# Optimization experiments

Hardware: AMD Instinct MI355X
Metric: run time of the kernel (lower is better)

## Reference

```python
import jax, jax.numpy as jnp
import numpy as np

A = 10      # n_trained_players = n_trained_off(5) + n_trained_def(5)
T = 65      # timesteps; scan runs T-1 = 64 steps
B = 128     # batch
XD, YD, ZD, HD, MD, RM = 2, 20, 64, 256, 90, 256
LOG2PI = float(np.log(2.0 * np.pi))


def _lin(x, W, b):
    # batched per-agent linear: x [A,B,in], W [A,in,out], b [A,out]
    return jnp.einsum('abi,aio->abo', x, W) + b[:, None, :]


def _mlp2(x, W1, b1, W2, b2):
    return jax.nn.relu(_lin(jax.nn.relu(_lin(x, W1, b1)), W2, b2))


def setup_inputs() -> dict:
    key = jax.random.key(0)
    ks = jax.random.split(key, 40)
    s = 0.05
    def w(i, shape):
        return jax.random.normal(ks[i], shape, dtype=jnp.float32) * s
    enc_in, pri_in, dec_in, gru_in = XD + MD + RM, MD + RM, YD + MD + ZD + RM, XD + ZD
    inp = {
        'data': jax.random.normal(ks[0], (T, B, YD), dtype=jnp.float32),
        'macro': jax.random.randint(ks[1], (T, B, A), 0, MD),
        'eps': jax.random.normal(ks[2], (T - 1, A, B, ZD), dtype=jnp.float32),
        'enc_W1': w(3, (A, enc_in, HD)), 'enc_b1': w(4, (A, HD)),
        'enc_W2': w(5, (A, HD, HD)), 'enc_b2': w(6, (A, HD)),
        'encm_W': w(7, (A, HD, ZD)), 'encm_b': w(8, (A, ZD)),
        'encs_W': w(9, (A, HD, ZD)), 'encs_b': w(10, (A, ZD)),
        'pri_W1': w(11, (A, pri_in, HD)), 'pri_b1': w(12, (A, HD)),
        'pri_W2': w(13, (A, HD, HD)), 'pri_b2': w(14, (A, HD)),
        'prim_W': w(15, (A, HD, ZD)), 'prim_b': w(16, (A, ZD)),
        'pris_W': w(17, (A, HD, ZD)), 'pris_b': w(18, (A, ZD)),
        'dec_W1': w(19, (A, dec_in, HD)), 'dec_b1': w(20, (A, HD)),
        'dec_W2': w(21, (A, HD, HD)), 'dec_b2': w(22, (A, HD)),
        'decm_W': w(23, (A, HD, XD)), 'decm_b': w(24, (A, XD)),
        'decs_W': w(25, (A, HD, XD)), 'decs_b': w(26, (A, XD)),
        'gru_Wih': w(27, (A, gru_in, 3 * RM)), 'gru_bih': w(28, (A, 3 * RM)),
        'gru_Whh': w(29, (A, RM, 3 * RM)), 'gru_bhh': w(30, (A, 3 * RM)),
    }
    return inp


def _forward(data, macro, eps, enc_W1, enc_b1, enc_W2, enc_b2, encm_W, encm_b,
             encs_W, encs_b, pri_W1, pri_b1, pri_W2, pri_b2, prim_W, prim_b,
             pris_W, pris_b, dec_W1, dec_b1, dec_W2, dec_b2, decm_W, decm_b,
             decs_W, decs_b, gru_Wih, gru_bih, gru_Whh, gru_bhh):
    # x: next-step per-player positions [T-1, A, B, 2]
    x = data[1:].reshape(T - 1, B, A, XD).transpose(0, 2, 1, 3)
    # macro one-hot, [T, A, B, 90]
    m = jax.nn.one_hot(macro, MD, dtype=data.dtype).transpose(0, 2, 1, 3)
    h0 = jnp.zeros((A, B, RM), data.dtype)
    zero = jnp.zeros((), data.dtype)

    def step(carry, ts):
        h, recon, kl = carry
        x_t, y_t, m_t, e_t = ts  # [A,B,2], [B,20], [A,B,90], [A,B,ZD]
        yb = jnp.broadcast_to(y_t[None], (A, B, YD))
        # encoder q(z|x,m,h)
        enc_h = _mlp2(jnp.concatenate([x_t, m_t, h], -1), enc_W1, enc_b1, enc_W2, enc_b2)
        enc_mean = _lin(enc_h, encm_W, encm_b)
        enc_std = jax.nn.softplus(_lin(enc_h, encs_W, encs_b))
        # prior p(z|m,h)
        pri_h = _mlp2(jnp.concatenate([m_t, h], -1), pri_W1, pri_b1, pri_W2, pri_b2)
        pri_mean = _lin(pri_h, prim_W, prim_b)
        pri_std = jax.nn.softplus(_lin(pri_h, pris_W, pris_b))
        # reparameterized sample
        z_t = enc_mean + e_t * enc_std
        # decoder p(x|y,m,z,h)
        dec_h = _mlp2(jnp.concatenate([yb, m_t, z_t, h], -1), dec_W1, dec_b1, dec_W2, dec_b2)
        dec_mean = _lin(dec_h, decm_W, decm_b)
        dec_std = jax.nn.softplus(_lin(dec_h, decs_W, decs_b))
        # per-agent 1-layer GRU (torch gate order: reset, update, new)
        gi = _lin(jnp.concatenate([x_t, z_t], -1), gru_Wih, gru_bih)
        gh = _lin(h, gru_Whh, gru_bhh)
        ir, iz, inn = jnp.split(gi, 3, axis=-1)
        hr, hz, hn = jnp.split(gh, 3, axis=-1)
        r = jax.nn.sigmoid(ir + hr)
        u = jax.nn.sigmoid(iz + hz)
        n = jnp.tanh(inn + r * hn)
        h_new = (1.0 - u) * n + u * h
        # losses (summed over all agents/batch/dims, as in torch code)
        kl = kl + 0.5 * jnp.sum(2.0 * jnp.log(pri_std) - 2.0 * jnp.log(enc_std)
                                + (enc_std ** 2 + (enc_mean - pri_mean) ** 2) / pri_std ** 2 - 1.0)
        recon = recon + jnp.sum(0.5 * ((x_t - dec_mean) / dec_std) ** 2
                                + jnp.log(dec_std) + 0.5 * LOG2PI)
        return (h_new, recon, kl), None

    xs = (x, data[:-1], m[:-1], eps)
    (_, recon, kl), _ = jax.lax.scan(step, (h0, zero, zero), xs)
    return recon, kl


def reference(data, macro, eps, enc_W1, enc_b1, enc_W2, enc_b2, encm_W, encm_b,
              encs_W, encs_b, pri_W1, pri_b1, pri_W2, pri_b2, prim_W, prim_b,
              pris_W, pris_b, dec_W1, dec_b1, dec_W2, dec_b2, decm_W, decm_b,
              decs_W, decs_b, gru_Wih, gru_bih, gru_Whh, gru_bhh):
    return _forward(data, macro, eps, enc_W1, enc_b1, enc_W2, enc_b2, encm_W, encm_b,
                    encs_W, encs_b, pri_W1, pri_b1, pri_W2, pri_b2, prim_W, prim_b,
                    pris_W, pris_b, dec_W1, dec_b1, dec_W2, dec_b2, decm_W, decm_b,
                    decs_W, decs_b, gru_Wih, gru_bih, gru_Whh, gru_bhh)
```

## Files before the change

kernel.cpp:

```cpp
#include <hip/hip_runtime.h>
#include <math.h>

#define NA 10
#define NT 65
#define NB 128
#define XDIM 2
#define YDIM 20
#define ZDIM 64
#define HDIM 256
#define RMDIM 256
#define NSTEP 64
#define TS 8
#define HR (TS + 1)
#define LOG2PI 1.8378770664093453f

#define ENC_W1_S (348 * 256)
#define PRI_W1_S (346 * 256)
#define DEC_W1_S (430 * 256)
#define GRU_WIH_S (66 * 768)
#define GRU_WHH_S (256 * 768)
#define W2_S (256 * 256)
#define HEADW_S (256 * 64)

#define SA (256 * NB)
#define GA (768 * NB)
#define ZA (ZDIM * NB)

static __device__ __forceinline__ float sp(float x) {
    return fmaxf(x, 0.f) + log1pf(expf(-fabsf(x)));
}
static __device__ __forceinline__ float sigm(float x) { return 1.f / (1.f + expf(-x)); }
static __device__ __forceinline__ float relu(float x) { return fmaxf(x, 0.f); }

__global__ __launch_bounds__(256) void k_init(float* __restrict__ h0, double* __restrict__ accd) {
    int i = blockIdx.x * 256 + threadIdx.x;
    ((float4*)h0)[i] = make_float4(0.f, 0.f, 0.f, 0.f);
    if (i == 0) {
        accd[0] = 0.0;
        accd[1] = 0.0;
    }
}

__global__ __launch_bounds__(256) void kS1(const float* __restrict__ h,
                                           const float* __restrict__ enc_W1,
                                           const float* __restrict__ enc_b1,
                                           const float* __restrict__ pri_W1,
                                           const float* __restrict__ pri_b1,
                                           const float* __restrict__ gru_Whh,
                                           const float* __restrict__ gru_bhh,
                                           const float* __restrict__ data,
                                           const int* __restrict__ macro, float* __restrict__ ench1,
                                           float* __restrict__ prih1, float* __restrict__ ghB,
                                           int t) {
    int tid = threadIdx.x, bid = blockIdx.x;
    int lane = tid & 63, wv = tid >> 6;
    int a = bid / 80;
    int r = bid % 80;
    int b0 = (r & 1) * 64;
    int tile = r >> 1;
    int ep, c0;
    const float* Wb;
    int wld;
    if (tile < 8) {
        ep = 0; c0 = tile * 32;
        Wb = enc_W1 + a * ENC_W1_S + 92 * 256; wld = 256;
    } else if (tile < 16) {
        ep = 1; c0 = (tile - 8) * 32;
        Wb = pri_W1 + a * PRI_W1_S + 90 * 256; wld = 256;
    } else {
        ep = 2; c0 = (tile - 16) * 32;
        Wb = gru_Whh + a * GRU_WHH_S; wld = 768;
    }
    int n0u = __builtin_amdgcn_readfirstlane(c0 + wv * 8);
    int row = b0 + lane;
    const float* X = h + a * SA + row;
    const float* wp = Wb + n0u;
    float acc[8] = {};
#pragma unroll 8
    for (int k = 0; k < 256; ++k) {
        float xv = X[k * NB];
        const float* wr = wp + k * wld;
#pragma unroll
        for (int j = 0; j < 8; ++j) acc[j] = fmaf(xv, wr[j], acc[j]);
    }
    if (ep == 2) {
#pragma unroll
        for (int j = 0; j < 8; ++j) {
            float v = acc[j] + gru_bhh[a * 768 + n0u + j];
            ghB[a * GA + (n0u + j) * NB + row] = v;
        }
    } else {
        const float* W1b = (ep == 0) ? enc_W1 + a * ENC_W1_S : pri_W1 + a * PRI_W1_S;
        const float* bb = (ep == 0) ? enc_b1 + a * HDIM : pri_b1 + a * HDIM;
        int mi = macro[(t * NB + row) * NA + a];
        const float* mrow = W1b + (ep == 0 ? 2 + mi : mi) * 256;
        float xv0 = 0.f, xv1 = 0.f;
        if (ep == 0) {
            xv0 = data[(t + 1) * (NB * YDIM) + row * YDIM + a * XDIM];
            xv1 = data[(t + 1) * (NB * YDIM) + row * YDIM + a * XDIM + 1];
        }
        float* outp = (ep == 0) ? ench1 : prih1;
#pragma unroll
        for (int j = 0; j < 8; ++j) {
            float v = acc[j] + bb[n0u + j] + mrow[n0u + j];
            if (ep == 0) v += xv0 * W1b[n0u + j] + xv1 * W1b[256 + n0u + j];
            outp[a * SA + (n0u + j) * NB + row] = relu(v);
        }
    }
}

__global__ __launch_bounds__(256) void kS2(const float* __restrict__ ench1,
                                           const float* __restrict__ prih1,
                                           const float* __restrict__ enc_W2,
                                           const float* __restrict__ enc_b2,
                                           const float* __restrict__ pri_W2,
                                           const float* __restrict__ pri_b2,
                                           float* __restrict__ ench2, float* __restrict__ prih2) {
    int tid = threadIdx.x, bid = blockIdx.x;
    int lane = tid & 63, wv = tid >> 6;
    int a = bid / 32;
    int r = bid % 32;
    int isenc = (r < 16);
    int q = isenc ? r : r - 16;
    int b0 = (q & 1) * 64;
    int c0 = (q >> 1) * 32;
    int n0u = __builtin_amdgcn_readfirstlane(c0 + wv * 8);
    int row = b0 + lane;
    const float* X = (isenc ? ench1 : prih1) + a * SA + row;
    const float* wp = (isenc ? enc_W2 : pri_W2) + a * W2_S + n0u;
    const float* bb = (isenc ? enc_b2 : pri_b2) + a * HDIM;
    float acc[8] = {};
#pragma unroll 8
    for (int k = 0; k < 256; ++k) {
        float xv = X[k * NB];
        const float* wr = wp + k * 256;
#pragma unroll
        for (int j = 0; j < 8; ++j) acc[j] = fmaf(xv, wr[j], acc[j]);
    }
    float* outp = isenc ? ench2 : prih2;
#pragma unroll
    for (int j = 0; j < 8; ++j)
        outp[a * SA + (n0u + j) * NB + row] = relu(acc[j] + bb[n0u + j]);
}

__global__ __launch_bounds__(256) void kS3(const float* __restrict__ ench2,
                                           const float* __restrict__ prih2,
                                           const float* __restrict__ encm_W,
                                           const float* __restrict__ encm_b,
                                           const float* __restrict__ encs_W,
                                           const float* __restrict__ encs_b,
                                           const float* __restrict__ prim_W,
                                           const float* __restrict__ prim_b,
                                           const float* __restrict__ pris_W,
                                           const float* __restrict__ pris_b,
                                           const float* __restrict__ eps, float* __restrict__ z_t,
                                           double* __restrict__ accd, int t) {
    __shared__ float L[4][16][64];
    __shared__ float red[256];
    int tid = threadIdx.x, bid = blockIdx.x;
    int lane = tid & 63, wv = tid >> 6;
    int a = bid / 8;
    int r = bid % 8;
    int b0 = (r & 1) * 64;
    int zc0 = (r >> 1) * 16;
    int row = b0 + lane;
    const float* Wt;
    const float* Bt;
    if (wv == 0) { Wt = encm_W; Bt = encm_b; }
    else if (wv == 1) { Wt = encs_W; Bt = encs_b; }
    else if (wv == 2) { Wt = prim_W; Bt = prim_b; }
    else { Wt = pris_W; Bt = pris_b; }
    const float* X = (wv < 2 ? ench2 : prih2) + a * SA + row;
    const float* wp = Wt + a * HEADW_S + zc0;
    float acc[16] = {};
#pragma unroll 4
    for (int k = 0; k < 256; ++k) {
        float xv = X[k * NB];
        const float* wr = wp + k * ZDIM;
#pragma unroll
        for (int j = 0; j < 16; ++j) acc[j] = fmaf(xv, wr[j], acc[j]);
    }
#pragma unroll
    for (int j = 0; j < 16; ++j) L[wv][j][lane] = acc[j] + Bt[a * ZDIM + zc0 + j];
    __syncthreads();
    float part = 0.f;
#pragma unroll
    for (int q = 0; q < 4; ++q) {
        int zc = wv * 4 + q;
        float em = L[0][zc][lane];
        float es = sp(L[1][zc][lane]);
        float pm = L[2][zc][lane];
        float ps = sp(L[3][zc][lane]);
        float ev = eps[((t * NA + a) * NB + row) * ZDIM + zc0 + zc];
        z_t[a * ZA + (zc0 + zc) * NB + row] = em + ev * es;
        float dm = em - pm;
        part += 0.5f * (2.f * logf(ps) - 2.f * logf(es) + (es * es + dm * dm) / (ps * ps) - 1.f);
    }
    red[tid] = part;
    __syncthreads();
#pragma unroll
    for (int s = 128; s > 0; s >>= 1) {
        if (tid < s) red[tid] += red[tid + s];
        __syncthreads();
    }
    if (tid == 0) atomicAdd(&accd[1], (double)red[0]);
}

__global__ __launch_bounds__(256) void kS4(const float* __restrict__ z_t,
                                           const float* __restrict__ data,
                                           const float* __restrict__ gru_Wih,
                                           const float* __restrict__ gru_bih,
                                           const float* __restrict__ ghB,
                                           const float* __restrict__ h_t, float* __restrict__ h_nx,
                                           int t) {
    int tid = threadIdx.x, bid = blockIdx.x;
    int lane = tid & 63, wv = tid >> 6;
    int a = bid / 16;
    int r = bid % 16;
    int b0 = (r & 1) * 64;
    int c0 = (r >> 1) * 32;
    int n0u = __builtin_amdgcn_readfirstlane(c0 + wv * 8);
    int row = b0 + lane;
    const float* X = z_t + a * ZA + row;
    const float* wp = gru_Wih + a * GRU_WIH_S + 2 * 768 + n0u;
    float acc[3][8] = {};
#pragma unroll 8
    for (int k = 0; k < 64; ++k) {
        float xv = X[k * NB];
        const float* wr = wp + k * 768;
#pragma unroll
        for (int j = 0; j < 8; ++j) acc[0][j] = fmaf(xv, wr[j], acc[0][j]);
#pragma unroll
        for (int j = 0; j < 8; ++j) acc[1][j] = fmaf(xv, wr[256 + j], acc[1][j]);
#pragma unroll
        for (int j = 0; j < 8; ++j) acc[2][j] = fmaf(xv, wr[512 + j], acc[2][j]);
    }
    float xv0 = data[(t + 1) * (NB * YDIM) + row * YDIM + a * XDIM];
    float xv1 = data[(t + 1) * (NB * YDIM) + row * YDIM + a * XDIM + 1];
    const float* Wih0 = gru_Wih + a * GRU_WIH_S;
    const float* bih = gru_bih + a * 768;
    const float* ghb = ghB + a * GA + row;
    const float* hb = h_t + a * SA + row;
    float* ob = h_nx + a * SA + row;
#pragma unroll
    for (int j = 0; j < 8; ++j) {
        int cr = n0u + j;
        float gi0 = acc[0][j] + bih[cr] + xv0 * Wih0[cr] + xv1 * Wih0[768 + cr];
        float gi1 = acc[1][j] + bih[256 + cr] + xv0 * Wih0[256 + cr] + xv1 * Wih0[768 + 256 + cr];
        float gi2 = acc[2][j] + bih[512 + cr] + xv0 * Wih0[512 + cr] + xv1 * Wih0[768 + 512 + cr];
        float hrv = ghb[cr * NB];
        float hzv = ghb[(256 + cr) * NB];
        float hnv = ghb[(512 + cr) * NB];
        float hov = hb[cr * NB];
        float rr = sigm(gi0 + hrv);
        float uu = sigm(gi1 + hzv);
        float nn = tanhf(gi2 + rr * hnv);
        ob[cr * NB] = (1.f - uu) * nn + uu * hov;
    }
}

__global__ __launch_bounds__(256) void kDec1(const float* __restrict__ data,
                                             const int* __restrict__ macro,
                                             const float* __restrict__ z_ring,
                                             const float* __restrict__ h_ring,
                                             const float* __restrict__ dec_W1,
                                             const float* __restrict__ dec_b1,
                                             float* __restrict__ dech1s, int t0) {
    int tid = threadIdx.x, bid = blockIdx.x;
    int lane = tid & 63, wv = tid >> 6;
    int ti = bid / 160;
    int rem = bid % 160;
    int a = rem / 16;
    int r = rem % 16;
    int b0 = (r & 1) * 64;
    int c0 = (r >> 1) * 32;
    int t = t0 + ti;
    int n0u = __builtin_amdgcn_readfirstlane(c0 + wv * 8);
    int row = b0 + lane;
    const float* Wb = dec_W1 + a * DEC_W1_S;
    const float* wp = Wb + n0u;
    float acc[8] = {};
    const float* yrow = data + t * (NB * YDIM) + row * YDIM;
#pragma unroll 4
    for (int k = 0; k < YDIM; ++k) {
        float xv = yrow[k];
        const float* wr = wp + k * 256;
#pragma unroll
        for (int j = 0; j < 8; ++j) acc[j] = fmaf(xv, wr[j], acc[j]);
    }
    const float* Xz = z_ring + (size_t)(t % TS) * (NA * ZA) + a * ZA + row;
#pragma unroll 8
    for (int k = 0; k < ZDIM; ++k) {
        float xv = Xz[k * NB];
        const float* wr = wp + (110 + k) * 256;
#pragma unroll
        for (int j = 0; j < 8; ++j) acc[j] = fmaf(xv, wr[j], acc[j]);
    }
    const float* Xh = h_ring + (size_t)(t % HR) * (NA * SA) + a * SA + row;
#pragma unroll 8
    for (int k = 0; k < 256; ++k) {
        float xv = Xh[k * NB];
        const float* wr = wp + (174 + k) * 256;
#pragma unroll
        for (int j = 0; j < 8; ++j) acc[j] = fmaf(xv, wr[j], acc[j]);
    }
    int mi = macro[(t * NB + row) * NA + a];
    const float* mrow = Wb + (20 + mi) * 256;
    const float* bb = dec_b1 + a * HDIM;
    float* ob = dech1s + (size_t)(ti * NA + a) * SA + row;
#pragma unroll
    for (int j = 0; j < 8; ++j)
        ob[(n0u + j) * NB] = relu(acc[j] + bb[n0u + j] + mrow[n0u + j]);
}

__global__ __launch_bounds__(256) void kDec2(const float* __restrict__ dech1s,
                                             const float* __restrict__ dec_W2,
                                             const float* __restrict__ dec_b2,
                                             float* __restrict__ dech2s) {
    int tid = threadIdx.x, bid = blockIdx.x;
    int lane = tid & 63, wv = tid >> 6;
    int ti = bid / 160;
    int rem = bid % 160;
    int a = rem / 16;
    int r = rem % 16;
    int b0 = (r & 1) * 64;
    int c0 = (r >> 1) * 32;
    int n0u = __builtin_amdgcn_readfirstlane(c0 + wv * 8);
    int row = b0 + lane;
    const float* X = dech1s + (size_t)(ti * NA + a) * SA + row;
    const float* wp = dec_W2 + a * W2_S + n0u;
    const float* bb = dec_b2 + a * HDIM;
    float acc[8] = {};
#pragma unroll 8
    for (int k = 0; k < 256; ++k) {
        float xv = X[k * NB];
        const float* wr = wp + k * 256;
#pragma unroll
        for (int j = 0; j < 8; ++j) acc[j] = fmaf(xv, wr[j], acc[j]);
    }
    float* ob = dech2s + (size_t)(ti * NA + a) * SA + row;
#pragma unroll
    for (int j = 0; j < 8; ++j)
        ob[(n0u + j) * NB] = relu(acc[j] + bb[n0u + j]);
}

__global__ __launch_bounds__(256) void kEpi(const float* __restrict__ dech2s,
                                            const float* __restrict__ decm_W,
                                            const float* __restrict__ decm_b,
                                            const float* __restrict__ decs_W,
                                            const float* __restrict__ decs_b,
                                            const float* __restrict__ data,
                                            double* __restrict__ accd, int t0) {
    int tid = threadIdx.x;
    int widx = blockIdx.x * 4 + (tid >> 6);
    int lane = tid & 63;
    int ti = widx / 1280;
    int rem = widx - ti * 1280;
    int a = rem >> 7, b = rem & 127;
    int targ = t0 + ti + 1;
    const float* dbase = dech2s + (size_t)(ti * NA + a) * SA + b;
    float hv0 = dbase[(lane * 4 + 0) * NB];
    float hv1 = dbase[(lane * 4 + 1) * NB];
    float hv2 = dbase[(lane * 4 + 2) * NB];
    float hv3 = dbase[(lane * 4 + 3) * NB];
    const float* wmb = decm_W + a * (HDIM * XDIM) + lane * 8;
    const float4 wm0 = *(const float4*)&wmb[0];
    const float4 wm1 = *(const float4*)&wmb[4];
    const float* wsb = decs_W + a * (HDIM * XDIM) + lane * 8;
    const float4 ws0 = *(const float4*)&wsb[0];
    const float4 ws1 = *(const float4*)&wsb[4];
    float m0 = hv0 * wm0.x + hv1 * wm0.z + hv2 * wm1.x + hv3 * wm1.z;
    float m1 = hv0 * wm0.y + hv1 * wm0.w + hv2 * wm1.y + hv3 * wm1.w;
    float s0 = hv0 * ws0.x + hv1 * ws0.z + hv2 * ws1.x + hv3 * ws1.z;
    float s1 = hv0 * ws0.y + hv1 * ws0.w + hv2 * ws1.y + hv3 * ws1.w;
#pragma unroll
    for (int off = 32; off > 0; off >>= 1) {
        m0 += __shfl_down(m0, off, 64);
        m1 += __shfl_down(m1, off, 64);
        s0 += __shfl_down(s0, off, 64);
        s1 += __shfl_down(s1, off, 64);
    }
    if (lane == 0) {
        float dm0 = m0 + decm_b[a * 2 + 0];
        float dm1 = m1 + decm_b[a * 2 + 1];
        float ds0 = sp(s0 + decs_b[a * 2 + 0]);
        float ds1 = sp(s1 + decs_b[a * 2 + 1]);
        float x0 = data[targ * (NB * YDIM) + b * YDIM + a * XDIM + 0];
        float x1 = data[targ * (NB * YDIM) + b * YDIM + a * XDIM + 1];
        float r0 = (x0 - dm0) / ds0, r1 = (x1 - dm1) / ds1;
        float tt = 0.5f * r0 * r0 + logf(ds0) + 0.5f * LOG2PI + 0.5f * r1 * r1 + logf(ds1) +
                   0.5f * LOG2PI;
        atomicAdd(&accd[0], (double)tt);
    }
}

__global__ void k_final(const double* __restrict__ accd, float* __restrict__ out) {
    if (threadIdx.x == 0) {
        out[0] = (float)accd[0];
        out[1] = (float)accd[1];
    }
}

extern "C" void kernel_launch(void* const* d_in, const int* in_sizes, int n_in, void* d_out,
                              int out_size, void* d_ws, size_t ws_size, hipStream_t stream) {
    const float* data = (const float*)d_in[0];
    const int* macro = (const int*)d_in[1];
    const float* eps = (const float*)d_in[2];
    const float* enc_W1 = (const float*)d_in[3];
    const float* enc_b1 = (const float*)d_in[4];
    const float* enc_W2 = (const float*)d_in[5];
    const float* enc_b2 = (const float*)d_in[6];
    const float* encm_W = (const float*)d_in[7];
    const float* encm_b = (const float*)d_in[8];
    const float* encs_W = (const float*)d_in[9];
    const float* encs_b = (const float*)d_in[10];
    const float* pri_W1 = (const float*)d_in[11];
    const float* pri_b1 = (const float*)d_in[12];
    const float* pri_W2 = (const float*)d_in[13];
    const float* pri_b2 = (const float*)d_in[14];
    const float* prim_W = (const float*)d_in[15];
    const float* prim_b = (const float*)d_in[16];
    const float* pris_W = (const float*)d_in[17];
    const float* pris_b = (const float*)d_in[18];
    const float* dec_W1 = (const float*)d_in[19];
    const float* dec_b1 = (const float*)d_in[20];
    const float* dec_W2 = (const float*)d_in[21];
    const float* dec_b2 = (const float*)d_in[22];
    const float* decm_W = (const float*)d_in[23];
    const float* decm_b = (const float*)d_in[24];
    const float* decs_W = (const float*)d_in[25];
    const float* decs_b = (const float*)d_in[26];
    const float* gru_Wih = (const float*)d_in[27];
    const float* gru_bih = (const float*)d_in[28];
    const float* gru_Whh = (const float*)d_in[29];
    const float* gru_bhh = (const float*)d_in[30];

    double* accd = (double*)d_ws;
    float* base = (float*)((char*)d_ws + 256);
    float* h_ring = base;
    float* z_ring = h_ring + (size_t)HR * NA * SA;
    float* ench1 = z_ring + (size_t)TS * NA * ZA;
    float* prih1 = ench1 + NA * SA;
    float* ench2 = prih1 + NA * SA;
    float* prih2 = ench2 + NA * SA;
    float* ghB = prih2 + NA * SA;
    float* dech1s = ghB + NA * GA;
    float* dech2s = dech1s + (size_t)TS * NA * SA;
    float* out = (float*)d_out;

    k_init<<<320, 256, 0, stream>>>(h_ring, accd);
    for (int t = 0; t < NSTEP; ++t) {
        float* h_t = h_ring + (size_t)(t % HR) * NA * SA;
        float* h_nx = h_ring + (size_t)((t + 1) % HR) * NA * SA;
        float* z_t = z_ring + (size_t)(t % TS) * NA * ZA;
        kS1<<<800, 256, 0, stream>>>(h_t, enc_W1, enc_b1, pri_W1, pri_b1, gru_Whh, gru_bhh, data,
                                     macro, ench1, prih1, ghB, t);
        kS2<<<320, 256, 0, stream>>>(ench1, prih1, enc_W2, enc_b2, pri_W2, pri_b2, ench2, prih2);
        kS3<<<80, 256, 0, stream>>>(ench2, prih2, encm_W, encm_b, encs_W, encs_b, prim_W, prim_b,
                                    pris_W, pris_b, eps, z_t, accd, t);
        kS4<<<160, 256, 0, stream>>>(z_t, data, gru_Wih, gru_bih, ghB, h_t, h_nx, t);
        if ((t % TS) == TS - 1) {
            int t0 = t - TS + 1;
            kDec1<<<TS * 160, 256, 0, stream>>>(data, macro, z_ring, h_ring, dec_W1, dec_b1,
                                                dech1s, t0);
            kDec2<<<TS * 160, 256, 0, stream>>>(dech1s, dec_W2, dec_b2, dech2s);
            kEpi<<<TS * 320, 256, 0, stream>>>(dech2s, decm_W, decm_b, decs_W, decs_b, data, accd,
                                               t0);
        }
    }
    k_final<<<1, 64, 0, stream>>>(accd, out);
}
```

Before: 11.29 ms.

## Replace per-step kernel launches with one persistent cooperative kernel using grid syncs

Merges all per-timestep kernels into a single cooperative persistent kernel that walks task lists and separates stages with grid-wide barriers, removing about 260 kernel launches. The decoder path is software-pipelined so each decoder step runs eight steps behind the scan, alongside scan work in the same phases, instead of in batched bursts. The latent heads are split into their own phase so more blocks share that work. The cost is grid.sync overhead per phase and occupancy limits from running a persistent grid.

```diff
diff --git a/kernel.cpp b/kernel.cpp
--- a/kernel.cpp
+++ b/kernel.cpp
@@ -1,5 +1,8 @@
 #include <hip/hip_runtime.h>
+#include <hip/hip_cooperative_groups.h>
 #include <math.h>
+
+namespace cg = cooperative_groups;
 
 #define NA 10
 #define NT 65
@@ -12,6 +15,7 @@
 #define NSTEP 64
 #define TS 8
 #define HR (TS + 1)
+#define MAXTASK 980
 #define LOG2PI 1.8378770664093453f
 
 #define ENC_W1_S (348 * 256)
@@ -32,30 +36,24 @@
 static __device__ __forceinline__ float sigm(float x) { return 1.f / (1.f + expf(-x)); }
 static __device__ __forceinline__ float relu(float x) { return fmaxf(x, 0.f); }
 
-__global__ __launch_bounds__(256) void k_init(float* __restrict__ h0, double* __restrict__ accd) {
-    int i = blockIdx.x * 256 + threadIdx.x;
-    ((float4*)h0)[i] = make_float4(0.f, 0.f, 0.f, 0.f);
-    if (i == 0) {
-        accd[0] = 0.0;
-        accd[1] = 0.0;
-    }
-}
-
-__global__ __launch_bounds__(256) void kS1(const float* __restrict__ h,
-                                           const float* __restrict__ enc_W1,
-                                           const float* __restrict__ enc_b1,
-                                           const float* __restrict__ pri_W1,
-                                           const float* __restrict__ pri_b1,
-                                           const float* __restrict__ gru_Whh,
-                                           const float* __restrict__ gru_bhh,
-                                           const float* __restrict__ data,
-                                           const int* __restrict__ macro, float* __restrict__ ench1,
-                                           float* __restrict__ prih1, float* __restrict__ ghB,
-                                           int t) {
-    int tid = threadIdx.x, bid = blockIdx.x;
-    int lane = tid & 63, wv = tid >> 6;
-    int a = bid / 80;
-    int r = bid % 80;
+struct Prm {
+    const float* data;
+    const int* macro;
+    const float* eps;
+    const float *enc_W1, *enc_b1, *enc_W2, *enc_b2, *encm_W, *encm_b, *encs_W, *encs_b;
+    const float *pri_W1, *pri_b1, *pri_W2, *pri_b2, *prim_W, *prim_b, *pris_W, *pris_b;
+    const float *dec_W1, *dec_b1, *dec_W2, *dec_b2, *decm_W, *decm_b, *decs_W, *decs_b;
+    const float *gWih, *gbih, *gWhh, *gbhh;
+    float *h_ring, *z_ring, *e1, *p1, *e2, *p2, *heads, *ghB, *dech1, *dech2;
+    double* accd;
+    float* out;
+};
+
+static __device__ __forceinline__ void task_l1(const Prm& p, int id, int t, const float* h_t) {
+    int tid = threadIdx.x;
+    int lane = tid & 63, wv = tid >> 6;
+    int a = id / 80;
+    int r = id % 80;
     int b0 = (r & 1) * 64;
     int tile = r >> 1;
     int ep, c0;
@@ -63,17 +61,17 @@
     int wld;
     if (tile < 8) {
         ep = 0; c0 = tile * 32;
-        Wb = enc_W1 + a * ENC_W1_S + 92 * 256; wld = 256;
+        Wb = p.enc_W1 + a * ENC_W1_S + 92 * 256; wld = 256;
     } else if (tile < 16) {
         ep = 1; c0 = (tile - 8) * 32;
-        Wb = pri_W1 + a * PRI_W1_S + 90 * 256; wld = 256;
+        Wb = p.pri_W1 + a * PRI_W1_S + 90 * 256; wld = 256;
     } else {
         ep = 2; c0 = (tile - 16) * 32;
-        Wb = gru_Whh + a * GRU_WHH_S; wld = 768;
-    }
-    int n0u = __builtin_amdgcn_readfirstlane(c0 + wv * 8);
-    int row = b0 + lane;
-    const float* X = h + a * SA + row;
+        Wb = p.gWhh + a * GRU_WHH_S; wld = 768;
+    }
+    int n0u = __builtin_amdgcn_readfirstlane(c0 + wv * 8);
+    int row = b0 + lane;
+    const float* X = h_t + a * SA + row;
     const float* wp = Wb + n0u;
     float acc[8] = {};
 #pragma unroll 8
@@ -85,21 +83,19 @@
     }
     if (ep == 2) {
 #pragma unroll
-        for (int j = 0; j < 8; ++j) {
-            float v = acc[j] + gru_bhh[a * 768 + n0u + j];
-            ghB[a * GA + (n0u + j) * NB + row] = v;
-        }
+        for (int j = 0; j < 8; ++j)
+            p.ghB[a * GA + (n0u + j) * NB + row] = acc[j] + p.gbhh[a * 768 + n0u + j];
     } else {
-        const float* W1b = (ep == 0) ? enc_W1 + a * ENC_W1_S : pri_W1 + a * PRI_W1_S;
-        const float* bb = (ep == 0) ? enc_b1 + a * HDIM : pri_b1 + a * HDIM;
-        int mi = macro[(t * NB + row) * NA + a];
+        const float* W1b = (ep == 0) ? p.enc_W1 + a * ENC_W1_S : p.pri_W1 + a * PRI_W1_S;
+        const float* bb = (ep == 0) ? p.enc_b1 + a * HDIM : p.pri_b1 + a * HDIM;
+        int mi = p.macro[(t * NB + row) * NA + a];
         const float* mrow = W1b + (ep == 0 ? 2 + mi : mi) * 256;
         float xv0 = 0.f, xv1 = 0.f;
         if (ep == 0) {
-            xv0 = data[(t + 1) * (NB * YDIM) + row * YDIM + a * XDIM];
-            xv1 = data[(t + 1) * (NB * YDIM) + row * YDIM + a * XDIM + 1];
-        }
-        float* outp = (ep == 0) ? ench1 : prih1;
+            xv0 = p.data[(t + 1) * (NB * YDIM) + row * YDIM + a * XDIM];
+            xv1 = p.data[(t + 1) * (NB * YDIM) + row * YDIM + a * XDIM + 1];
+        }
+        float* outp = (ep == 0) ? p.e1 : p.p1;
 #pragma unroll
         for (int j = 0; j < 8; ++j) {
             float v = acc[j] + bb[n0u + j] + mrow[n0u + j];
@@ -109,26 +105,111 @@
     }
 }
 
-__global__ __launch_bounds__(256) void kS2(const float* __restrict__ ench1,
-                                           const float* __restrict__ prih1,
-                                           const float* __restrict__ enc_W2,
-                                           const float* __restrict__ enc_b2,
-                                           const float* __restrict__ pri_W2,
-                                           const float* __restrict__ pri_b2,
-                                           float* __restrict__ ench2, float* __restrict__ prih2) {
-    int tid = threadIdx.x, bid = blockIdx.x;
-    int lane = tid & 63, wv = tid >> 6;
-    int a = bid / 32;
-    int r = bid % 32;
-    int isenc = (r < 16);
-    int q = isenc ? r : r - 16;
+static __device__ __forceinline__ void task_dec1(const Prm& p, int q, int tD) {
+    int tid = threadIdx.x;
+    int lane = tid & 63, wv = tid >> 6;
+    int a = q / 16;
+    int r = q % 16;
+    int b0 = (r & 1) * 64;
+    int c0 = (r >> 1) * 32;
+    int n0u = __builtin_amdgcn_readfirstlane(c0 + wv * 8);
+    int row = b0 + lane;
+    const float* Wb = p.dec_W1 + a * DEC_W1_S;
+    const float* wp = Wb + n0u;
+    float acc[8] = {};
+    const float* yrow = p.data + tD * (NB * YDIM) + row * YDIM;
+#pragma unroll 4
+    for (int k = 0; k < YDIM; ++k) {
+        float xv = yrow[k];
+        const float* wr = wp + k * 256;
+#pragma unroll
+        for (int j = 0; j < 8; ++j) acc[j] = fmaf(xv, wr[j], acc[j]);
+    }
+    const float* Xz = p.z_ring + (size_t)(tD % TS) * (NA * ZA) + a * ZA + row;
+#pragma unroll 8
+    for (int k = 0; k < ZDIM; ++k) {
+        float xv = Xz[k * NB];
+        const float* wr = wp + (110 + k) * 256;
+#pragma unroll
+        for (int j = 0; j < 8; ++j) acc[j] = fmaf(xv, wr[j], acc[j]);
+    }
+    const float* Xh = p.h_ring + (size_t)(tD % HR) * (NA * SA) + a * SA + row;
+#pragma unroll 8
+    for (int k = 0; k < 256; ++k) {
+        float xv = Xh[k * NB];
+        const float* wr = wp + (174 + k) * 256;
+#pragma unroll
+        for (int j = 0; j < 8; ++j) acc[j] = fmaf(xv, wr[j], acc[j]);
+    }
+    int mi = p.macro[(tD * NB + row) * NA + a];
+    const float* mrow = Wb + (20 + mi) * 256;
+    const float* bb = p.dec_b1 + a * HDIM;
+    float* ob = p.dech1 + a * SA + row;
+#pragma unroll
+    for (int j = 0; j < 8; ++j)
+        ob[(n0u + j) * NB] = relu(acc[j] + bb[n0u + j] + mrow[n0u + j]);
+}
+
+static __device__ __forceinline__ void task_epi(const Prm& p, int q, int tE, float* Ls) {
+    int tid = threadIdx.x;
+    int lane = tid & 63, wv = tid >> 6;
+    int a = q >> 1;
     int b0 = (q & 1) * 64;
-    int c0 = (q >> 1) * 32;
-    int n0u = __builtin_amdgcn_readfirstlane(c0 + wv * 8);
-    int row = b0 + lane;
-    const float* X = (isenc ? ench1 : prih1) + a * SA + row;
-    const float* wp = (isenc ? enc_W2 : pri_W2) + a * W2_S + n0u;
-    const float* bb = (isenc ? enc_b2 : pri_b2) + a * HDIM;
+    int row = b0 + lane;
+    const float* d2 = p.dech2 + a * SA;
+    const float* wm = p.decm_W + a * (HDIM * XDIM);
+    const float* ws = p.decs_W + a * (HDIM * XDIM);
+    float m0 = 0.f, m1 = 0.f, s0 = 0.f, s1 = 0.f;
+#pragma unroll 8
+    for (int kk = 0; kk < 64; ++kk) {
+        int k = wv * 64 + kk;
+        float xv = d2[k * NB + row];
+        m0 = fmaf(xv, wm[k * 2], m0);
+        m1 = fmaf(xv, wm[k * 2 + 1], m1);
+        s0 = fmaf(xv, ws[k * 2], s0);
+        s1 = fmaf(xv, ws[k * 2 + 1], s1);
+    }
+    Ls[(wv * 4 + 0) * 64 + lane] = m0;
+    Ls[(wv * 4 + 1) * 64 + lane] = m1;
+    Ls[(wv * 4 + 2) * 64 + lane] = s0;
+    Ls[(wv * 4 + 3) * 64 + lane] = s1;
+    __syncthreads();
+    if (wv == 0) {
+        float M0 = Ls[0 * 64 + lane] + Ls[4 * 64 + lane] + Ls[8 * 64 + lane] + Ls[12 * 64 + lane];
+        float M1 = Ls[1 * 64 + lane] + Ls[5 * 64 + lane] + Ls[9 * 64 + lane] + Ls[13 * 64 + lane];
+        float S0 = Ls[2 * 64 + lane] + Ls[6 * 64 + lane] + Ls[10 * 64 + lane] + Ls[14 * 64 + lane];
+        float S1 = Ls[3 * 64 + lane] + Ls[7 * 64 + lane] + Ls[11 * 64 + lane] + Ls[15 * 64 + lane];
+        float dm0 = M0 + p.decm_b[a * 2 + 0];
+        float dm1 = M1 + p.decm_b[a * 2 + 1];
+        float ds0 = sp(S0 + p.decs_b[a * 2 + 0]);
+        float ds1 = sp(S1 + p.decs_b[a * 2 + 1]);
+        int targ = tE + 1;
+        float x0 = p.data[targ * (NB * YDIM) + row * YDIM + a * XDIM + 0];
+        float x1 = p.data[targ * (NB * YDIM) + row * YDIM + a * XDIM + 1];
+        float r0 = (x0 - dm0) / ds0, r1 = (x1 - dm1) / ds1;
+        float tt = 0.5f * r0 * r0 + logf(ds0) + 0.5f * LOG2PI + 0.5f * r1 * r1 + logf(ds1) +
+                   0.5f * LOG2PI;
+#pragma unroll
+        for (int off = 32; off > 0; off >>= 1) tt += __shfl_down(tt, off, 64);
+        if (lane == 0) atomicAdd(&p.accd[0], (double)tt);
+    }
+    __syncthreads();
+}
+
+static __device__ __forceinline__ void task_l2(const Prm& p, int id) {
+    int tid = threadIdx.x;
+    int lane = tid & 63, wv = tid >> 6;
+    int isenc = (id < 160);
+    int q = isenc ? id : id - 160;
+    int a = q / 16;
+    int r = q % 16;
+    int b0 = (r & 1) * 64;
+    int c0 = (r >> 1) * 32;
+    int n0u = __builtin_amdgcn_readfirstlane(c0 + wv * 8);
+    int row = b0 + lane;
+    const float* X = (isenc ? p.e1 : p.p1) + a * SA + row;
+    const float* wp = (isenc ? p.enc_W2 : p.pri_W2) + a * W2_S + n0u;
+    const float* bb = (isenc ? p.enc_b2 : p.pri_b2) + a * HDIM;
     float acc[8] = {};
 #pragma unroll 8
     for (int k = 0; k < 256; ++k) {
@@ -137,96 +218,118 @@
 #pragma unroll
         for (int j = 0; j < 8; ++j) acc[j] = fmaf(xv, wr[j], acc[j]);
     }
-    float* outp = isenc ? ench2 : prih2;
+    float* outp = isenc ? p.e2 : p.p2;
 #pragma unroll
     for (int j = 0; j < 8; ++j)
         outp[a * SA + (n0u + j) * NB + row] = relu(acc[j] + bb[n0u + j]);
 }
 
-__global__ __launch_bounds__(256) void kS3(const float* __restrict__ ench2,
-                                           const float* __restrict__ prih2,
-                                           const float* __restrict__ encm_W,
-                                           const float* __restrict__ encm_b,
-                                           const float* __restrict__ encs_W,
-                                           const float* __restrict__ encs_b,
-                                           const float* __restrict__ prim_W,
-                                           const float* __restrict__ prim_b,
-                                           const float* __restrict__ pris_W,
-                                           const float* __restrict__ pris_b,
-                                           const float* __restrict__ eps, float* __restrict__ z_t,
-                                           double* __restrict__ accd, int t) {
-    __shared__ float L[4][16][64];
-    __shared__ float red[256];
-    int tid = threadIdx.x, bid = blockIdx.x;
-    int lane = tid & 63, wv = tid >> 6;
-    int a = bid / 8;
-    int r = bid % 8;
-    int b0 = (r & 1) * 64;
-    int zc0 = (r >> 1) * 16;
-    int row = b0 + lane;
+static __device__ __forceinline__ void task_dec2(const Prm& p, int q) {
+    int tid = threadIdx.x;
+    int lane = tid & 63, wv = tid >> 6;
+    int a = q / 16;
+    int r = q % 16;
+    int b0 = (r & 1) * 64;
+    int c0 = (r >> 1) * 32;
+    int n0u = __builtin_amdgcn_readfirstlane(c0 + wv * 8);
+    int row = b0 + lane;
+    const float* X = p.dech1 + a * SA + row;
+    const float* wp = p.dec_W2 + a * W2_S + n0u;
+    const float* bb = p.dec_b2 + a * HDIM;
+    float acc[8] = {};
+#pragma unroll 8
+    for (int k = 0; k < 256; ++k) {
+        float xv = X[k * NB];
+        const float* wr = wp + k * 256;
+#pragma unroll
+        for (int j = 0; j < 8; ++j) acc[j] = fmaf(xv, wr[j], acc[j]);
+    }
+    float* ob = p.dech2 + a * SA + row;
+#pragma unroll
+    for (int j = 0; j < 8; ++j)
+        ob[(n0u + j) * NB] = relu(acc[j] + bb[n0u + j]);
+}
+
+static __device__ __forceinline__ void task_heads(const Prm& p, int id) {
+    int tid = threadIdx.x;
+    int lane = tid & 63, wv = tid >> 6;
+    int a = id / 16;
+    int r = id % 16;
+    int b0 = (r & 1) * 64;
+    int hc = r >> 1;
+    int head = hc >> 1, c0 = (hc & 1) * 32;
     const float* Wt;
     const float* Bt;
-    if (wv == 0) { Wt = encm_W; Bt = encm_b; }
-    else if (wv == 1) { Wt = encs_W; Bt = encs_b; }
-    else if (wv == 2) { Wt = prim_W; Bt = prim_b; }
-    else { Wt = pris_W; Bt = pris_b; }
-    const float* X = (wv < 2 ? ench2 : prih2) + a * SA + row;
-    const float* wp = Wt + a * HEADW_S + zc0;
-    float acc[16] = {};
-#pragma unroll 4
+    if (head == 0) { Wt = p.encm_W; Bt = p.encm_b; }
+    else if (head == 1) { Wt = p.encs_W; Bt = p.encs_b; }
+    else if (head == 2) { Wt = p.prim_W; Bt = p.prim_b; }
+    else { Wt = p.pris_W; Bt = p.pris_b; }
+    int n0u = __builtin_amdgcn_readfirstlane(c0 + wv * 8);
+    int row = b0 + lane;
+    const float* X = (head < 2 ? p.e2 : p.p2) + a * SA + row;
+    const float* wp = Wt + a * HEADW_S + n0u;
+    float acc[8] = {};
+#pragma unroll 8
     for (int k = 0; k < 256; ++k) {
         float xv = X[k * NB];
         const float* wr = wp + k * ZDIM;
 #pragma unroll
-        for (int j = 0; j < 16; ++j) acc[j] = fmaf(xv, wr[j], acc[j]);
-    }
-#pragma unroll
-    for (int j = 0; j < 16; ++j) L[wv][j][lane] = acc[j] + Bt[a * ZDIM + zc0 + j];
+        for (int j = 0; j < 8; ++j) acc[j] = fmaf(xv, wr[j], acc[j]);
+    }
+#pragma unroll
+    for (int j = 0; j < 8; ++j)
+        p.heads[a * SA + (head * 64 + n0u + j) * NB + row] = acc[j] + Bt[a * ZDIM + n0u + j];
+}
+
+static __device__ __forceinline__ void task_p4(const Prm& p, int id, int t, const float* h_t,
+                                               float* h_nx, float* z_t, float* Ls, float* red) {
+    int tid = threadIdx.x;
+    int lane = tid & 63, wv = tid >> 6;
+    int a = id / 16;
+    int r = id % 16;
+    int b0 = (r & 1) * 64;
+    int c0 = (r >> 1) * 32;
+    int n0u = __builtin_amdgcn_readfirstlane(c0 + wv * 8);
+    const float* heads_a = p.heads + a * SA;
+    {
+        int rl = tid & 63, zg = tid >> 6;
+        int rg = b0 + rl;
+        float part = 0.f;
+#pragma unroll 4
+        for (int i = 0; i < 16; ++i) {
+            int zc = zg * 16 + i;
+            float em = heads_a[zc * NB + rg];
+            float esr = heads_a[(64 + zc) * NB + rg];
+            float es = sp(esr);
+            float e = p.eps[((size_t)(t * NA + a) * NB + rg) * ZDIM + zc];
+            float zv = em + e * es;
+            Ls[zc * 64 + rl] = zv;
+            if (c0 == 0) z_t[a * ZA + zc * NB + rg] = zv;
+            if (c0 == 32) {
+                float pm = heads_a[(128 + zc) * NB + rg];
+                float ps = sp(heads_a[(192 + zc) * NB + rg]);
+                float dm = em - pm;
+                part += 0.5f * (2.f * logf(ps) - 2.f * logf(es) +
+                                (es * es + dm * dm) / (ps * ps) - 1.f);
+            }
+        }
+        if (c0 == 32) red[tid] = part;
+    }
     __syncthreads();
-    float part = 0.f;
-#pragma unroll
-    for (int q = 0; q < 4; ++q) {
-        int zc = wv * 4 + q;
-        float em = L[0][zc][lane];
-        float es = sp(L[1][zc][lane]);
-        float pm = L[2][zc][lane];
-        float ps = sp(L[3][zc][lane]);
-        float ev = eps[((t * NA + a) * NB + row) * ZDIM + zc0 + zc];
-        z_t[a * ZA + (zc0 + zc) * NB + row] = em + ev * es;
-        float dm = em - pm;
-        part += 0.5f * (2.f * logf(ps) - 2.f * logf(es) + (es * es + dm * dm) / (ps * ps) - 1.f);
-    }
-    red[tid] = part;
-    __syncthreads();
-#pragma unroll
-    for (int s = 128; s > 0; s >>= 1) {
-        if (tid < s) red[tid] += red[tid + s];
+    if (c0 == 32) {
+#pragma unroll
+        for (int s = 128; s > 0; s >>= 1) {
+            if (tid < s) red[tid] += red[tid + s];
+            __syncthreads();
+        }
+        if (tid == 0) atomicAdd(&p.accd[1], (double)red[0]);
         __syncthreads();
     }
-    if (tid == 0) atomicAdd(&accd[1], (double)red[0]);
-}
-
-__global__ __launch_bounds__(256) void kS4(const float* __restrict__ z_t,
-                                           const float* __restrict__ data,
-                                           const float* __restrict__ gru_Wih,
-                                           const float* __restrict__ gru_bih,
-                                           const float* __restrict__ ghB,
-                                           const float* __restrict__ h_t, float* __restrict__ h_nx,
-                                           int t) {
-    int tid = threadIdx.x, bid = blockIdx.x;
-    int lane = tid & 63, wv = tid >> 6;
-    int a = bid / 16;
-    int r = bid % 16;
-    int b0 = (r & 1) * 64;
-    int c0 = (r >> 1) * 32;
-    int n0u = __builtin_amdgcn_readfirstlane(c0 + wv * 8);
-    int row = b0 + lane;
-    const float* X = z_t + a * ZA + row;
-    const float* wp = gru_Wih + a * GRU_WIH_S + 2 * 768 + n0u;
     float acc[3][8] = {};
+    const float* wp = p.gWih + a * GRU_WIH_S + 2 * 768 + n0u;
 #pragma unroll 8
     for (int k = 0; k < 64; ++k) {
-        float xv = X[k * NB];
+        float xv = Ls[k * 64 + lane];
         const float* wr = wp + k * 768;
 #pragma unroll
         for (int j = 0; j < 8; ++j) acc[0][j] = fmaf(xv, wr[j], acc[0][j]);
@@ -235,11 +338,12 @@
 #pragma unroll
         for (int j = 0; j < 8; ++j) acc[2][j] = fmaf(xv, wr[512 + j], acc[2][j]);
     }
-    float xv0 = data[(t + 1) * (NB * YDIM) + row * YDIM + a * XDIM];
-    float xv1 = data[(t + 1) * (NB * YDIM) + row * YDIM + a * XDIM + 1];
-    const float* Wih0 = gru_Wih + a * GRU_WIH_S;
-    const float* bih = gru_bih + a * 768;
-    const float* ghb = ghB + a * GA + row;
+    int row = b0 + lane;
+    float xv0 = p.data[(t + 1) * (NB * YDIM) + row * YDIM + a * XDIM];
+    float xv1 = p.data[(t + 1) * (NB * YDIM) + row * YDIM + a * XDIM + 1];
+    const float* Wih0 = p.gWih + a * GRU_WIH_S;
+    const float* bih = p.gbih + a * 768;
+    const float* ghb = p.ghB + a * GA + row;
     const float* hb = h_t + a * SA + row;
     float* ob = h_nx + a * SA + row;
 #pragma unroll
@@ -257,216 +361,113 @@
         float nn = tanhf(gi2 + rr * hnv);
         ob[cr * NB] = (1.f - uu) * nn + uu * hov;
     }
-}
-
-__global__ __launch_bounds__(256) void kDec1(const float* __restrict__ data,
-                                             const int* __restrict__ macro,
-                                             const float* __restrict__ z_ring,
-                                             const float* __restrict__ h_ring,
-                                             const float* __restrict__ dec_W1,
-                                             const float* __restrict__ dec_b1,
-                                             float* __restrict__ dech1s, int t0) {
-    int tid = threadIdx.x, bid = blockIdx.x;
-    int lane = tid & 63, wv = tid >> 6;
-    int ti = bid / 160;
-    int rem = bid % 160;
-    int a = rem / 16;
-    int r = rem % 16;
-    int b0 = (r & 1) * 64;
-    int c0 = (r >> 1) * 32;
-    int t = t0 + ti;
-    int n0u = __builtin_amdgcn_readfirstlane(c0 + wv * 8);
-    int row = b0 + lane;
-    const float* Wb = dec_W1 + a * DEC_W1_S;
-    const float* wp = Wb + n0u;
-    float acc[8] = {};
-    const float* yrow = data + t * (NB * YDIM) + row * YDIM;
-#pragma unroll 4
-    for (int k = 0; k < YDIM; ++k) {
-        float xv = yrow[k];
-        const float* wr = wp + k * 256;
-#pragma unroll
-        for (int j = 0; j < 8; ++j) acc[j] = fmaf(xv, wr[j], acc[j]);
-    }
-    const float* Xz = z_ring + (size_t)(t % TS) * (NA * ZA) + a * ZA + row;
-#pragma unroll 8
-    for (int k = 0; k < ZDIM; ++k) {
-        float xv = Xz[k * NB];
-        const float* wr = wp + (110 + k) * 256;
-#pragma unroll
-        for (int j = 0; j < 8; ++j) acc[j] = fmaf(xv, wr[j], acc[j]);
-    }
-    const float* Xh = h_ring + (size_t)(t % HR) * (NA * SA) + a * SA + row;
-#pragma unroll 8
-    for (int k = 0; k < 256; ++k) {
-        float xv = Xh[k * NB];
-        const float* wr = wp + (174 + k) * 256;
-#pragma unroll
-        for (int j = 0; j < 8; ++j) acc[j] = fmaf(xv, wr[j], acc[j]);
-    }
-    int mi = macro[(t * NB + row) * NA + a];
-    const float* mrow = Wb + (20 + mi) * 256;
-    const float* bb = dec_b1 + a * HDIM;
-    float* ob = dech1s + (size_t)(ti * NA + a) * SA + row;
-#pragma unroll
-    for (int j = 0; j < 8; ++j)
-        ob[(n0u + j) * NB] = relu(acc[j] + bb[n0u + j] + mrow[n0u + j]);
-}
-
-__global__ __launch_bounds__(256) void kDec2(const float* __restrict__ dech1s,
-                                             const float* __restrict__ dec_W2,
-                                             const float* __restrict__ dec_b2,
-                                             float* __restrict__ dech2s) {
-    int tid = threadIdx.x, bid = blockIdx.x;
-    int lane = tid & 63, wv = tid >> 6;
-    int ti = bid / 160;
-    int rem = bid % 160;
-    int a = rem / 16;
-    int r = rem % 16;
-    int b0 = (r & 1) * 64;
-    int c0 = (r >> 1) * 32;
-    int n0u = __builtin_amdgcn_readfirstlane(c0 + wv * 8);
-    int row = b0 + lane;
-    const float* X = dech1s + (size_t)(ti * NA + a) * SA + row;
-    const float* wp = dec_W2 + a * W2_S + n0u;
-    const float* bb = dec_b2 + a * HDIM;
-    float acc[8] = {};
-#pragma unroll 8
-    for (int k = 0; k < 256; ++k) {
-        float xv = X[k * NB];
-        const float* wr = wp + k * 256;
-#pragma unroll
-        for (int j = 0; j < 8; ++j) acc[j] = fmaf(xv, wr[j], acc[j]);
-    }
-    float* ob = dech2s + (size_t)(ti * NA + a) * SA + row;
-#pragma unroll
-    for (int j = 0; j < 8; ++j)
-        ob[(n0u + j) * NB] = relu(acc[j] + bb[n0u + j]);
-}
-
-__global__ __launch_bounds__(256) void kEpi(const float* __restrict__ dech2s,
-                                            const float* __restrict__ decm_W,
-                                            const float* __restrict__ decm_b,
-                                            const float* __restrict__ decs_W,
-                                            const float* __restrict__ decs_b,
-                                            const float* __restrict__ data,
-                                            double* __restrict__ accd, int t0) {
-    int tid = threadIdx.x;
-    int widx = blockIdx.x * 4 + (tid >> 6);
-    int lane = tid & 63;
-    int ti = widx / 1280;
-    int rem = widx - ti * 1280;
-    int a = rem >> 7, b = rem & 127;
-    int targ = t0 + ti + 1;
-    const float* dbase = dech2s + (size_t)(ti * NA + a) * SA + b;
-    float hv0 = dbase[(lane * 4 + 0) * NB];
-    float hv1 = dbase[(lane * 4 + 1) * NB];
-    float hv2 = dbase[(lane * 4 + 2) * NB];
-    float hv3 = dbase[(lane * 4 + 3) * NB];
-    const float* wmb = decm_W + a * (HDIM * XDIM) + lane * 8;
-    const float4 wm0 = *(const float4*)&wmb[0];
-    const float4 wm1 = *(const float4*)&wmb[4];
-    const float* wsb = decs_W + a * (HDIM * XDIM) + lane * 8;
-    const float4 ws0 = *(const float4*)&wsb[0];
-    const float4 ws1 = *(const float4*)&wsb[4];
-    float m0 = hv0 * wm0.x + hv1 * wm0.z + hv2 * wm1.x + hv3 * wm1.z;
-    float m1 = hv0 * wm0.y + hv1 * wm0.w + hv2 * wm1.y + hv3 * wm1.w;
-    float s0 = hv0 * ws0.x + hv1 * ws0.z + hv2 * ws1.x + hv3 * ws1.z;
-    float s1 = hv0 * ws0.y + hv1 * ws0.w + hv2 * ws1.y + hv3 * ws1.w;
-#pragma unroll
-    for (int off = 32; off > 0; off >>= 1) {
-        m0 += __shfl_down(m0, off, 64);
-        m1 += __shfl_down(m1, off, 64);
-        s0 += __shfl_down(s0, off, 64);
-        s1 += __shfl_down(s1, off, 64);
-    }
-    if (lane == 0) {
-        float dm0 = m0 + decm_b[a * 2 + 0];
-        float dm1 = m1 + decm_b[a * 2 + 1];
-        float ds0 = sp(s0 + decs_b[a * 2 + 0]);
-        float ds1 = sp(s1 + decs_b[a * 2 + 1]);
-        float x0 = data[targ * (NB * YDIM) + b * YDIM + a * XDIM + 0];
-        float x1 = data[targ * (NB * YDIM) + b * YDIM + a * XDIM + 1];
-        float r0 = (x0 - dm0) / ds0, r1 = (x1 - dm1) / ds1;
-        float tt = 0.5f * r0 * r0 + logf(ds0) + 0.5f * LOG2PI + 0.5f * r1 * r1 + logf(ds1) +
-                   0.5f * LOG2PI;
-        atomicAdd(&accd[0], (double)tt);
-    }
-}
-
-__global__ void k_final(const double* __restrict__ accd, float* __restrict__ out) {
-    if (threadIdx.x == 0) {
-        out[0] = (float)accd[0];
-        out[1] = (float)accd[1];
+    __syncthreads();
+}
+
+__global__ __launch_bounds__(256, 4) void kmain(Prm p) {
+    cg::grid_group grid = cg::this_grid();
+    const int tid = threadIdx.x, bid = blockIdx.x;
+    const int nb = gridDim.x;
+    __shared__ float Ls[64 * 64];
+    __shared__ float red[256];
+    {
+        int g0 = bid * 256 + tid;
+        float4* h0 = (float4*)p.h_ring;
+        for (int i = g0; i < (NA * SA) / 4; i += nb * 256)
+            h0[i] = make_float4(0.f, 0.f, 0.f, 0.f);
+        if (g0 == 0) { p.accd[0] = 0.0; p.accd[1] = 0.0; }
+    }
+    grid.sync();
+    for (int t = 0; t <= NSTEP + 8; ++t) {
+        const float* h_t = p.h_ring + (size_t)(t % HR) * NA * SA;
+        float* h_nx = p.h_ring + (size_t)((t + 1) % HR) * NA * SA;
+        float* z_t = p.z_ring + (size_t)(t % TS) * NA * ZA;
+        int tD = t - 8, tE = t - 9;
+        int nScan = (t < NSTEP) ? 800 : 0;
+        int nD1 = (tD >= 0 && tD < NSTEP) ? 160 : 0;
+        int nEpi = (tE >= 0 && tE < NSTEP) ? 20 : 0;
+        for (int id = bid; id < nScan + nD1 + nEpi; id += nb) {
+            if (id < nScan) task_l1(p, id, t, h_t);
+            else if (id < nScan + nD1) task_dec1(p, id - nScan, tD);
+            else task_epi(p, id - nScan - nD1, tE, Ls);
+        }
+        grid.sync();
+        int nL2 = (t < NSTEP) ? 320 : 0;
+        int nD2 = nD1;
+        for (int id = bid; id < nL2 + nD2; id += nb) {
+            if (id < nL2) task_l2(p, id);
+            else task_dec2(p, id - nL2);
+        }
+        grid.sync();
+        if (t < NSTEP) {
+            for (int id = bid; id < 160; id += nb) task_heads(p, id);
+            grid.sync();
+            for (int id = bid; id < 160; id += nb)
+                task_p4(p, id, t, h_t, h_nx, z_t, Ls, red);
+            grid.sync();
+        }
+    }
+    if (bid == 0 && tid == 0) {
+        p.out[0] = (float)p.accd[0];
+        p.out[1] = (float)p.accd[1];
     }
 }
 
 extern "C" void kernel_launch(void* const* d_in, const int* in_sizes, int n_in, void* d_out,
                               int out_size, void* d_ws, size_t ws_size, hipStream_t stream) {
-    const float* data = (const float*)d_in[0];
-    const int* macro = (const int*)d_in[1];
-    const float* eps = (const float*)d_in[2];
-    const float* enc_W1 = (const float*)d_in[3];
-    const float* enc_b1 = (const float*)d_in[4];
-    const float* enc_W2 = (const float*)d_in[5];
-    const float* enc_b2 = (const float*)d_in[6];
-    const float* encm_W = (const float*)d_in[7];
-    const float* encm_b = (const float*)d_in[8];
-    const float* encs_W = (const float*)d_in[9];
-    const float* encs_b = (const float*)d_in[10];
-    const float* pri_W1 = (const float*)d_in[11];
-    const float* pri_b1 = (const float*)d_in[12];
-    const float* pri_W2 = (const float*)d_in[13];
-    const float* pri_b2 = (const float*)d_in[14];
-    const float* prim_W = (const float*)d_in[15];
-    const float* prim_b = (const float*)d_in[16];
-    const float* pris_W = (const float*)d_in[17];
-    const float* pris_b = (const float*)d_in[18];
-    const float* dec_W1 = (const float*)d_in[19];
-    const float* dec_b1 = (const float*)d_in[20];
-    const float* dec_W2 = (const float*)d_in[21];
-    const float* dec_b2 = (const float*)d_in[22];
-    const float* decm_W = (const float*)d_in[23];
-    const float* decm_b = (const float*)d_in[24];
-    const float* decs_W = (const float*)d_in[25];
-    const float* decs_b = (const float*)d_in[26];
-    const float* gru_Wih = (const float*)d_in[27];
-    const float* gru_bih = (const float*)d_in[28];
-    const float* gru_Whh = (const float*)d_in[29];
-    const float* gru_bhh = (const float*)d_in[30];
-
-    double* accd = (double*)d_ws;
+    Prm p;
+    p.data = (const float*)d_in[0];
+    p.macro = (const int*)d_in[1];
+    p.eps = (const float*)d_in[2];
+    p.enc_W1 = (const float*)d_in[3];
+    p.enc_b1 = (const float*)d_in[4];
+    p.enc_W2 = (const float*)d_in[5];
+    p.enc_b2 = (const float*)d_in[6];
+    p.encm_W = (const float*)d_in[7];
+    p.encm_b = (const float*)d_in[8];
+    p.encs_W = (const float*)d_in[9];
+    p.encs_b = (const float*)d_in[10];
+    p.pri_W1 = (const float*)d_in[11];
+    p.pri_b1 = (const float*)d_in[12];
+    p.pri_W2 = (const float*)d_in[13];
+    p.pri_b2 = (const float*)d_in[14];
+    p.prim_W = (const float*)d_in[15];
+    p.prim_b = (const float*)d_in[16];
+    p.pris_W = (const float*)d_in[17];
+    p.pris_b = (const float*)d_in[18];
+    p.dec_W1 = (const float*)d_in[19];
+    p.dec_b1 = (const float*)d_in[20];
+    p.dec_W2 = (const float*)d_in[21];
+    p.dec_b2 = (const float*)d_in[22];
+    p.decm_W = (const float*)d_in[23];
+    p.decm_b = (const float*)d_in[24];
+    p.decs_W = (const float*)d_in[25];
+    p.decs_b = (const float*)d_in[26];
+    p.gWih = (const float*)d_in[27];
+    p.gbih = (const float*)d_in[28];
+    p.gWhh = (const float*)d_in[29];
+    p.gbhh = (const float*)d_in[30];
+
+    p.accd = (double*)d_ws;
     float* base = (float*)((char*)d_ws + 256);
-    float* h_ring = base;
-    float* z_ring = h_ring + (size_t)HR * NA * SA;
-    float* ench1 = z_ring + (size_t)TS * NA * ZA;
-    float* prih1 = ench1 + NA * SA;
-    float* ench2 = prih1 + NA * SA;
-    float* prih2 = ench2 + NA * SA;
-    float* ghB = prih2 + NA * SA;
-    float* dech1s = ghB + NA * GA;
-    float* dech2s = dech1s + (size_t)TS * NA * SA;
-    float* out = (float*)d_out;
-
-    k_init<<<320, 256, 0, stream>>>(h_ring, accd);
-    for (int t = 0; t < NSTEP; ++t) {
-        float* h_t = h_ring + (size_t)(t % HR) * NA * SA;
-        float* h_nx = h_ring + (size_t)((t + 1) % HR) * NA * SA;
-        float* z_t = z_ring + (size_t)(t % TS) * NA * ZA;
-        kS1<<<800, 256, 0, stream>>>(h_t, enc_W1, enc_b1, pri_W1, pri_b1, gru_Whh, gru_bhh, data,
-                                     macro, ench1, prih1, ghB, t);
-        kS2<<<320, 256, 0, stream>>>(ench1, prih1, enc_W2, enc_b2, pri_W2, pri_b2, ench2, prih2);
-        kS3<<<80, 256, 0, stream>>>(ench2, prih2, encm_W, encm_b, encs_W, encs_b, prim_W, prim_b,
-                                    pris_W, pris_b, eps, z_t, accd, t);
-        kS4<<<160, 256, 0, stream>>>(z_t, data, gru_Wih, gru_bih, ghB, h_t, h_nx, t);
-        if ((t % TS) == TS - 1) {
-            int t0 = t - TS + 1;
-            kDec1<<<TS * 160, 256, 0, stream>>>(data, macro, z_ring, h_ring, dec_W1, dec_b1,
-                                                dech1s, t0);
-            kDec2<<<TS * 160, 256, 0, stream>>>(dech1s, dec_W2, dec_b2, dech2s);
-            kEpi<<<TS * 320, 256, 0, stream>>>(dech2s, decm_W, decm_b, decs_W, decs_b, data, accd,
-                                               t0);
-        }
-    }
-    k_final<<<1, 64, 0, stream>>>(accd, out);
-}
+    p.h_ring = base;
+    p.z_ring = p.h_ring + (size_t)HR * NA * SA;
+    p.e1 = p.z_ring + (size_t)TS * NA * ZA;
+    p.p1 = p.e1 + NA * SA;
+    p.e2 = p.p1 + NA * SA;
+    p.p2 = p.e2 + NA * SA;
+    p.heads = p.p2 + NA * SA;
+    p.ghB = p.heads + NA * SA;
+    p.dech1 = p.ghB + (size_t)NA * GA;
+    p.dech2 = p.dech1 + NA * SA;
+    p.out = (float*)d_out;
+
+    int bpc = 0;
+    hipOccupancyMaxActiveBlocksPerMultiprocessor(&bpc, (const void*)kmain, 256, 0);
+    if (bpc < 1) bpc = 1;
+    int grid = bpc * 256;
+    if (grid > MAXTASK) grid = MAXTASK;
+
+    void* args[] = {&p};
+    hipLaunchCooperativeKernel((void*)kmain, dim3(grid), dim3(256), args, 0, stream);
+}
```

New measurement: 39.75 ms. 252% more time.
